# Kernel optimization log

Measured on AMD Instinct MI355X. Metric: run time of the kernel, lower is better.

Reference implementation:

```python
import jax, jax.numpy as jnp
import numpy as np

M, L, D, V = 4096, 15, 1024, 32  # moves, word_max, in_sz, vocab_sz


def setup_inputs() -> dict:
    key = jax.random.key(0)
    ks = jax.random.split(key, 9)
    s = 0.02
    return {
        "tokens": jax.random.randint(ks[0], (M, L), 0, V),
        "letter_emb": jax.random.normal(ks[1], (V, D), jnp.float32) * s,
        "pos_emb": jax.random.normal(ks[2], (L, D), jnp.float32) * s,
        "Wq": jax.random.normal(ks[3], (D, D), jnp.float32) * s,
        "bq": jax.random.normal(ks[4], (D,), jnp.float32) * s,
        "Wk": jax.random.normal(ks[5], (D, D), jnp.float32) * s,
        "bk": jax.random.normal(ks[6], (D,), jnp.float32) * s,
        "Wv": jax.random.normal(ks[7], (D, D), jnp.float32) * s,
        "bv": jax.random.normal(ks[8], (D,), jnp.float32) * s,
    }


def reference(tokens, letter_emb, pos_emb, Wq, bq, Wk, bk, Wv, bv):
    # WordEncoder, batched across all M moves.
    x = letter_emb[tokens] + pos_emb[None, :, :]          # [M, L, D]
    q = jnp.einsum("mld,ed->mle", x, Wq) + bq             # Linear: x @ W.T + b
    k = jnp.einsum("mld,ed->mle", x, Wk) + bk
    v = jnp.einsum("mld,ed->mle", x, Wv) + bv
    scores = jax.nn.softmax(jnp.einsum("mle,mke->mlk", q, k), axis=-1)  # [M, L, L]
    attn = jnp.einsum("mlk,mke->mle", scores, v)          # [M, L, D]
    word = attn.sum(axis=1)                               # [M, D]
    # enc = word + ordered, where ordered is an identical second evaluation
    # of word_enc on the same word -> enc = 2 * word.
    return 2.0 * word
```

## Files before the change

kernel.cpp:

```cpp
#include <hip/hip_runtime.h>
#include <hip/hip_bf16.h>

#define NMOVES 4096
#define LW     15
#define DIM    1024
#define VOC    32
#define NROW   480
#define MROW   512

#define GSPLIT 4
#define KSEG   (DIM/GSPLIT)
#define GN     512

typedef __attribute__((ext_vector_type(8))) short  short8;
typedef __attribute__((ext_vector_type(4))) float  floatx4;

__device__ __forceinline__ unsigned short f2b(float f) {
  unsigned int x;
  __builtin_memcpy(&x, &f, 4);
  x = x + 0x7FFFu + ((x >> 16) & 1u);
  return (unsigned short)(x >> 16);
}
__device__ __forceinline__ float b2f(unsigned short u) {
  unsigned int x = ((unsigned int)u) << 16;
  float f;
  __builtin_memcpy(&f, &x, 4);
  return f;
}

#define LDK 72

__global__ __launch_bounds__(256) void prep(
    const float* __restrict__ letter, const float* __restrict__ pos,
    const float* __restrict__ Wq, const float* __restrict__ Wk,
    const float* __restrict__ Wv,
    unsigned short* __restrict__ Eb, unsigned short* __restrict__ Wb) {
  const int id = blockIdx.x * 256 + threadIdx.x;
  const int ECHUNK = MROW * DIM / 8;
  const int WCHUNK = DIM * DIM / 8;

  if (id < ECHUNK) {
    const int row = id >> 7;
    const int c   = (id & 127) << 3;
    ushort4 o0 = make_ushort4(0, 0, 0, 0), o1 = o0;
    if (row < NROW) {
      const int t = row / LW;
      const int l = row - t * LW;
      const float* la = letter + (size_t)t * DIM + c;
      const float* lp = pos    + (size_t)l * DIM + c;
      float4 x0 = *reinterpret_cast<const float4*>(la);
      float4 x1 = *reinterpret_cast<const float4*>(la + 4);
      float4 p0 = *reinterpret_cast<const float4*>(lp);
      float4 p1 = *reinterpret_cast<const float4*>(lp + 4);
      o0.x = f2b(x0.x + p0.x); o0.y = f2b(x0.y + p0.y);
      o0.z = f2b(x0.z + p0.z); o0.w = f2b(x0.w + p0.w);
      o1.x = f2b(x1.x + p1.x); o1.y = f2b(x1.y + p1.y);
      o1.z = f2b(x1.z + p1.z); o1.w = f2b(x1.w + p1.w);
    }
    *reinterpret_cast<ushort4*>(Eb + (size_t)row * DIM + c)     = o0;
    *reinterpret_cast<ushort4*>(Eb + (size_t)row * DIM + c + 4) = o1;
  } else {
    const int wi = id - ECHUNK;
    const int m  = wi >> 17;
    const int rem = wi & (WCHUNK - 1);
    const float* src = (m == 0) ? Wq : (m == 1) ? Wk : Wv;
    const float* p = src + (size_t)rem * 8;
    float4 x0 = *reinterpret_cast<const float4*>(p);
    float4 x1 = *reinterpret_cast<const float4*>(p + 4);
    ushort4 o0, o1;
    o0.x = f2b(x0.x); o0.y = f2b(x0.y); o0.z = f2b(x0.z); o0.w = f2b(x0.w);
    o1.x = f2b(x1.x); o1.y = f2b(x1.y); o1.z = f2b(x1.z); o1.w = f2b(x1.w);
    unsigned short* dst = Wb + (size_t)m * DIM * DIM + (size_t)rem * 8;
    *reinterpret_cast<ushort4*>(dst)     = o0;
    *reinterpret_cast<ushort4*>(dst + 4) = o1;
  }
}

__global__ __launch_bounds__(256) void qkv_fused(
    const unsigned short* __restrict__ Eb, const unsigned short* __restrict__ Wb,
    const float* __restrict__ bq, const float* __restrict__ bk,
    const float* __restrict__ bv,
    unsigned short* __restrict__ Qb, unsigned short* __restrict__ Kb,
    unsigned short* __restrict__ Vb) {
  __shared__ __attribute__((aligned(16))) unsigned short lA[64 * LDK];
  __shared__ __attribute__((aligned(16))) unsigned short lB[64 * LDK];

  const unsigned short* W = Wb + (size_t)blockIdx.z * DIM * DIM;
  const float* bias = (blockIdx.z == 0) ? bq : (blockIdx.z == 1) ? bk : bv;
  unsigned short* O = (blockIdx.z == 0) ? Qb : (blockIdx.z == 1) ? Kb : Vb;

  const int bm0 = blockIdx.x * 64;
  const int bn0 = blockIdx.y * 64;

  const int tid  = threadIdx.x;
  const int lane = tid & 63;
  const int wave = tid >> 6;
  const int wr   = wave >> 1;
  const int wc   = wave & 1;
  const int quad = lane >> 4;
  const int l16  = lane & 15;

  const int srow = tid >> 3;
  const int scol = (tid & 7) << 3;

  const unsigned short* As = Eb + (size_t)(bm0 + srow) * DIM + scol;
  const unsigned short* Bs = W  + (size_t)(bn0 + srow) * DIM + scol;

  short8 ra0 = *reinterpret_cast<const short8*>(As);
  short8 ra1 = *reinterpret_cast<const short8*>(As + 32 * DIM);
  short8 rb0 = *reinterpret_cast<const short8*>(Bs);
  short8 rb1 = *reinterpret_cast<const short8*>(Bs + 32 * DIM);

  floatx4 acc[2][2];
#pragma unroll
  for (int i = 0; i < 2; ++i)
#pragma unroll
    for (int j = 0; j < 2; ++j) acc[i][j] = (floatx4){0.f, 0.f, 0.f, 0.f};

  for (int k0 = 0; k0 < DIM; k0 += 64) {
    *reinterpret_cast<short8*>(lA + srow * LDK + scol)        = ra0;
    *reinterpret_cast<short8*>(lA + (srow + 32) * LDK + scol) = ra1;
    *reinterpret_cast<short8*>(lB + srow * LDK + scol)        = rb0;
    *reinterpret_cast<short8*>(lB + (srow + 32) * LDK + scol) = rb1;
    __syncthreads();
    if (k0 + 64 < DIM) {
      ra0 = *reinterpret_cast<const short8*>(As + k0 + 64);
      ra1 = *reinterpret_cast<const short8*>(As + 32 * DIM + k0 + 64);
      rb0 = *reinterpret_cast<const short8*>(Bs + k0 + 64);
      rb1 = *reinterpret_cast<const short8*>(Bs + 32 * DIM + k0 + 64);
    }
#pragma unroll
    for (int kk = 0; kk < 64; kk += 32) {
      short8 a0 = *reinterpret_cast<const short8*>(lA + (wr * 32 + l16) * LDK + kk + quad * 8);
      short8 a1 = *reinterpret_cast<const short8*>(lA + (wr * 32 + 16 + l16) * LDK + kk + quad * 8);
      short8 b0 = *reinterpret_cast<const short8*>(lB + (wc * 32 + l16) * LDK + kk + quad * 8);
      short8 b1 = *reinterpret_cast<const short8*>(lB + (wc * 32 + 16 + l16) * LDK + kk + quad * 8);
      acc[0][0] = __builtin_amdgcn_mfma_f32_16x16x32_bf16(a0, b0, acc[0][0], 0, 0, 0);
      acc[0][1] = __builtin_amdgcn_mfma_f32_16x16x32_bf16(a0, b1, acc[0][1], 0, 0, 0);
      acc[1][0] = __builtin_amdgcn_mfma_f32_16x16x32_bf16(a1, b0, acc[1][0], 0, 0, 0);
      acc[1][1] = __builtin_amdgcn_mfma_f32_16x16x32_bf16(a1, b1, acc[1][1], 0, 0, 0);
    }
    __syncthreads();
  }

#pragma unroll
  for (int mi = 0; mi < 2; ++mi) {
#pragma unroll
    for (int ni = 0; ni < 2; ++ni) {
      const int gcol = bn0 + wc * 32 + ni * 16 + l16;
      const float bval = bias[gcol];
#pragma unroll
      for (int i = 0; i < 4; ++i) {
        const int grow = bm0 + wr * 32 + mi * 16 + quad * 4 + i;
        O[(size_t)grow * DIM + gcol] = f2b(acc[mi][ni][i] + bval);
      }
    }
  }
}

__global__ __launch_bounds__(256) void gram_split(
    const unsigned short* __restrict__ Qb, const unsigned short* __restrict__ Kb,
    float* __restrict__ Gpart) {
  __shared__ __attribute__((aligned(16))) unsigned short lA[64 * LDK];
  __shared__ __attribute__((aligned(16))) unsigned short lB[64 * LDK];

  const int bm0 = blockIdx.x * 64;
  const int bn0 = blockIdx.y * 64;
  const int kbase = blockIdx.z * KSEG;
  float* Gout = Gpart + (size_t)blockIdx.z * GN * GN;

  const int tid  = threadIdx.x;
  const int lane = tid & 63;
  const int wave = tid >> 6;
  const int wr   = wave >> 1;
  const int wc   = wave & 1;
  const int quad = lane >> 4;
  const int l16  = lane & 15;
  const int srow = tid >> 3;
  const int scol = (tid & 7) << 3;

  const unsigned short* As = Qb + (size_t)(bm0 + srow) * DIM + kbase + scol;
  const unsigned short* Bs = Kb + (size_t)(bn0 + srow) * DIM + kbase + scol;

  short8 ra0 = *reinterpret_cast<const short8*>(As);
  short8 ra1 = *reinterpret_cast<const short8*>(As + 32 * DIM);
  short8 rb0 = *reinterpret_cast<const short8*>(Bs);
  short8 rb1 = *reinterpret_cast<const short8*>(Bs + 32 * DIM);

  floatx4 acc[2][2];
#pragma unroll
  for (int i = 0; i < 2; ++i)
#pragma unroll
    for (int j = 0; j < 2; ++j) acc[i][j] = (floatx4){0.f, 0.f, 0.f, 0.f};

  for (int k0 = 0; k0 < KSEG; k0 += 64) {
    *reinterpret_cast<short8*>(lA + srow * LDK + scol)        = ra0;
    *reinterpret_cast<short8*>(lA + (srow + 32) * LDK + scol) = ra1;
    *reinterpret_cast<short8*>(lB + srow * LDK + scol)        = rb0;
    *reinterpret_cast<short8*>(lB + (srow + 32) * LDK + scol) = rb1;
    __syncthreads();
    if (k0 + 64 < KSEG) {
      ra0 = *reinterpret_cast<const short8*>(As + k0 + 64);
      ra1 = *reinterpret_cast<const short8*>(As + 32 * DIM + k0 + 64);
      rb0 = *reinterpret_cast<const short8*>(Bs + k0 + 64);
      rb1 = *reinterpret_cast<const short8*>(Bs + 32 * DIM + k0 + 64);
    }
#pragma unroll
    for (int kk = 0; kk < 64; kk += 32) {
      short8 a0 = *reinterpret_cast<const short8*>(lA + (wr * 32 + l16) * LDK + kk + quad * 8);
      short8 a1 = *reinterpret_cast<const short8*>(lA + (wr * 32 + 16 + l16) * LDK + kk + quad * 8);
      short8 b0 = *reinterpret_cast<const short8*>(lB + (wc * 32 + l16) * LDK + kk + quad * 8);
      short8 b1 = *reinterpret_cast<const short8*>(lB + (wc * 32 + 16 + l16) * LDK + kk + quad * 8);
      acc[0][0] = __builtin_amdgcn_mfma_f32_16x16x32_bf16(a0, b0, acc[0][0], 0, 0, 0);
      acc[0][1] = __builtin_amdgcn_mfma_f32_16x16x32_bf16(a0, b1, acc[0][1], 0, 0, 0);
      acc[1][0] = __builtin_amdgcn_mfma_f32_16x16x32_bf16(a1, b0, acc[1][0], 0, 0, 0);
      acc[1][1] = __builtin_amdgcn_mfma_f32_16x16x32_bf16(a1, b1, acc[1][1], 0, 0, 0);
    }
    __syncthreads();
  }

#pragma unroll
  for (int mi = 0; mi < 2; ++mi) {
#pragma unroll
    for (int ni = 0; ni < 2; ++ni) {
      const int gcol = bn0 + wc * 32 + ni * 16 + l16;
#pragma unroll
      for (int i = 0; i < 4; ++i) {
        const int grow = bm0 + wr * 32 + mi * 16 + quad * 4 + i;
        Gout[(size_t)grow * GN + gcol] = acc[mi][ni][i];
      }
    }
  }
}

__global__ __launch_bounds__(256) void attn_out_k(
    const void* __restrict__ tokens_raw, const float* __restrict__ Gpart,
    const unsigned short* __restrict__ Vb, float* __restrict__ out) {
  __shared__ int   ridx[LW];
  __shared__ float S[LW][16];
  __shared__ float w[16];
  __shared__ int   is64_s;
  const int m = blockIdx.x;
  const int tid = threadIdx.x;

  const unsigned int* u32 = (const unsigned int*)tokens_raw;
  if (tid < 64) {
    unsigned int v = u32[2 * tid + 1];
    unsigned long long nz = __ballot(v != 0);
    if (tid == 0) is64_s = (nz == 0ULL) ? 1 : 0;
  }
  __syncthreads();

  if (tid < LW) {
    int t;
    if (is64_s) t = (int)((const long long*)tokens_raw)[m * LW + tid];
    else        t = ((const int*)tokens_raw)[m * LW + tid];
    ridx[tid] = t * LW + tid;
  }
  __syncthreads();

  if (tid < LW * LW) {
    const int l = tid / LW;
    const int j = tid - l * LW;
    const size_t off = (size_t)ridx[l] * GN + ridx[j];
    float s = 0.f;
#pragma unroll
    for (int p = 0; p < GSPLIT; ++p) s += Gpart[(size_t)p * GN * GN + off];
    S[l][j] = s;
  }
  __syncthreads();

  if (tid < LW) {
    float mx = -1e30f;
#pragma unroll
    for (int j = 0; j < LW; ++j) mx = fmaxf(mx, S[tid][j]);
    float s = 0.f;
#pragma unroll
    for (int j = 0; j < LW; ++j) { float e = __expf(S[tid][j] - mx); S[tid][j] = e; s += e; }
    const float inv = 1.0f / s;
#pragma unroll
    for (int j = 0; j < LW; ++j) S[tid][j] *= inv;
  }
  __syncthreads();

  if (tid < LW) {
    float s = 0.f;
#pragma unroll
    for (int l = 0; l < LW; ++l) s += S[l][tid];
    w[tid] = 2.0f * s;
  }
  __syncthreads();

  const int e0 = tid * 4;
  float a0 = 0.f, a1 = 0.f, a2 = 0.f, a3 = 0.f;
#pragma unroll
  for (int j = 0; j < LW; ++j) {
    const float wj = w[j];
    ushort4 vv = *reinterpret_cast<const ushort4*>(Vb + (size_t)ridx[j] * DIM + e0);
    a0 += wj * b2f(vv.x);
    a1 += wj * b2f(vv.y);
    a2 += wj * b2f(vv.z);
    a3 += wj * b2f(vv.w);
  }
  *reinterpret_cast<float4*>(out + (size_t)m * DIM + e0) =
      make_float4(a0, a1, a2, a3);
}

extern "C" void kernel_launch(void* const* d_in, const int* in_sizes, int n_in,
                              void* d_out, int out_size, void* d_ws, size_t ws_size,
                              hipStream_t stream) {
  const void*  tokens = d_in[0];
  const float* letter = (const float*)d_in[1];
  const float* pos    = (const float*)d_in[2];
  const float* Wq     = (const float*)d_in[3];
  const float* bq     = (const float*)d_in[4];
  const float* Wk     = (const float*)d_in[5];
  const float* bk     = (const float*)d_in[6];
  const float* Wv     = (const float*)d_in[7];
  const float* bv     = (const float*)d_in[8];
  float*       outp   = (float*)d_out;

  char* ws = (char*)d_ws;
  const size_t EB_SZ = (size_t)MROW * DIM * 2;
  const size_t WB_SZ = (size_t)3 * DIM * DIM * 2;
  const size_t OB_SZ = (size_t)MROW * DIM * 2;
  unsigned short* Eb = (unsigned short*)(ws);
  unsigned short* Wb = (unsigned short*)(ws + EB_SZ);
  unsigned short* Qb = (unsigned short*)(ws + EB_SZ + WB_SZ);
  unsigned short* Kb = (unsigned short*)(ws + EB_SZ + WB_SZ + OB_SZ);
  unsigned short* Vb = (unsigned short*)(ws + EB_SZ + WB_SZ + 2 * OB_SZ);
  float*          Gp = (float*)(ws + EB_SZ + WB_SZ + 3 * OB_SZ);

  const int ECHUNK = MROW * DIM / 8;
  const int WCHUNK = DIM * DIM / 8;
  const int PREP_BLOCKS = (ECHUNK + 3 * WCHUNK) / 256;

  prep<<<PREP_BLOCKS, 256, 0, stream>>>(letter, pos, Wq, Wk, Wv, Eb, Wb);
  qkv_fused<<<dim3(8, 16, 3), 256, 0, stream>>>(Eb, Wb, bq, bk, bv, Qb, Kb, Vb);
  gram_split<<<dim3(8, 8, GSPLIT), 256, 0, stream>>>(Qb, Kb, Gp);
  attn_out_k<<<NMOVES, 256, 0, stream>>>(tokens, Gp, Vb, outp);
}
```

Before: 124.9 us.

## Project letter and position embeddings separately and build a 48-row Gram basis

Instead of materialising 480 embedding rows and projecting them through full Q/K/V GEMMs, the kernel projects only the 32 letter rows and 15 position rows, reading fp32 weights and converting to bf16 on the fly. A single block then forms a 48x48 Gram matrix that includes a bias row. The attention kernel rebuilds each score from six basis entries. Terms that are constant across the softmax axis (query·bk, bq·bk) are dropped, which is valid because softmax ignores them. V rows are expanded from the basis plus bias in the same launch. This removes the weight-conversion pass and most GEMM work, but the Gram step now runs serially on one block.

```diff
diff --git a/kernel.cpp b/kernel.cpp
--- a/kernel.cpp
+++ b/kernel.cpp
@@ -6,11 +6,8 @@
 #define DIM    1024
 #define VOC    32
 #define NROW   480
-#define MROW   512
-
-#define GSPLIT 4
-#define KSEG   (DIM/GSPLIT)
-#define GN     512
+#define XROW   48
+#define G48LD  64
 
 typedef __attribute__((ext_vector_type(8))) short  short8;
 typedef __attribute__((ext_vector_type(4))) float  floatx4;
@@ -21,6 +18,10 @@
   x = x + 0x7FFFu + ((x >> 16) & 1u);
   return (unsigned short)(x >> 16);
 }
+__device__ __forceinline__ ushort4 cvt4(float4 v) {
+  ushort4 o; o.x = f2b(v.x); o.y = f2b(v.y); o.z = f2b(v.z); o.w = f2b(v.w);
+  return o;
+}
 __device__ __forceinline__ float b2f(unsigned short u) {
   unsigned int x = ((unsigned int)u) << 16;
   float f;
@@ -30,66 +31,17 @@
 
 #define LDK 72
 
-__global__ __launch_bounds__(256) void prep(
+__global__ __launch_bounds__(256) void proj_small(
     const float* __restrict__ letter, const float* __restrict__ pos,
     const float* __restrict__ Wq, const float* __restrict__ Wk,
     const float* __restrict__ Wv,
-    unsigned short* __restrict__ Eb, unsigned short* __restrict__ Wb) {
-  const int id = blockIdx.x * 256 + threadIdx.x;
-  const int ECHUNK = MROW * DIM / 8;
-  const int WCHUNK = DIM * DIM / 8;
-
-  if (id < ECHUNK) {
-    const int row = id >> 7;
-    const int c   = (id & 127) << 3;
-    ushort4 o0 = make_ushort4(0, 0, 0, 0), o1 = o0;
-    if (row < NROW) {
-      const int t = row / LW;
-      const int l = row - t * LW;
-      const float* la = letter + (size_t)t * DIM + c;
-      const float* lp = pos    + (size_t)l * DIM + c;
-      float4 x0 = *reinterpret_cast<const float4*>(la);
-      float4 x1 = *reinterpret_cast<const float4*>(la + 4);
-      float4 p0 = *reinterpret_cast<const float4*>(lp);
-      float4 p1 = *reinterpret_cast<const float4*>(lp + 4);
-      o0.x = f2b(x0.x + p0.x); o0.y = f2b(x0.y + p0.y);
-      o0.z = f2b(x0.z + p0.z); o0.w = f2b(x0.w + p0.w);
-      o1.x = f2b(x1.x + p1.x); o1.y = f2b(x1.y + p1.y);
-      o1.z = f2b(x1.z + p1.z); o1.w = f2b(x1.w + p1.w);
-    }
-    *reinterpret_cast<ushort4*>(Eb + (size_t)row * DIM + c)     = o0;
-    *reinterpret_cast<ushort4*>(Eb + (size_t)row * DIM + c + 4) = o1;
-  } else {
-    const int wi = id - ECHUNK;
-    const int m  = wi >> 17;
-    const int rem = wi & (WCHUNK - 1);
-    const float* src = (m == 0) ? Wq : (m == 1) ? Wk : Wv;
-    const float* p = src + (size_t)rem * 8;
-    float4 x0 = *reinterpret_cast<const float4*>(p);
-    float4 x1 = *reinterpret_cast<const float4*>(p + 4);
-    ushort4 o0, o1;
-    o0.x = f2b(x0.x); o0.y = f2b(x0.y); o0.z = f2b(x0.z); o0.w = f2b(x0.w);
-    o1.x = f2b(x1.x); o1.y = f2b(x1.y); o1.z = f2b(x1.z); o1.w = f2b(x1.w);
-    unsigned short* dst = Wb + (size_t)m * DIM * DIM + (size_t)rem * 8;
-    *reinterpret_cast<ushort4*>(dst)     = o0;
-    *reinterpret_cast<ushort4*>(dst + 4) = o1;
-  }
-}
-
-__global__ __launch_bounds__(256) void qkv_fused(
-    const unsigned short* __restrict__ Eb, const unsigned short* __restrict__ Wb,
-    const float* __restrict__ bq, const float* __restrict__ bk,
-    const float* __restrict__ bv,
-    unsigned short* __restrict__ Qb, unsigned short* __restrict__ Kb,
-    unsigned short* __restrict__ Vb) {
+    float* __restrict__ Xq, float* __restrict__ Xk, float* __restrict__ Xv) {
   __shared__ __attribute__((aligned(16))) unsigned short lA[64 * LDK];
   __shared__ __attribute__((aligned(16))) unsigned short lB[64 * LDK];
 
-  const unsigned short* W = Wb + (size_t)blockIdx.z * DIM * DIM;
-  const float* bias = (blockIdx.z == 0) ? bq : (blockIdx.z == 1) ? bk : bv;
-  unsigned short* O = (blockIdx.z == 0) ? Qb : (blockIdx.z == 1) ? Kb : Vb;
-
-  const int bm0 = blockIdx.x * 64;
+  const float* W = (blockIdx.z == 0) ? Wq : (blockIdx.z == 1) ? Wk : Wv;
+  float*       O = (blockIdx.z == 0) ? Xq : (blockIdx.z == 1) ? Xk : Xv;
+
   const int bn0 = blockIdx.y * 64;
 
   const int tid  = threadIdx.x;
@@ -99,17 +51,24 @@
   const int wc   = wave & 1;
   const int quad = lane >> 4;
   const int l16  = lane & 15;
-
   const int srow = tid >> 3;
   const int scol = (tid & 7) << 3;
 
-  const unsigned short* As = Eb + (size_t)(bm0 + srow) * DIM + scol;
-  const unsigned short* Bs = W  + (size_t)(bn0 + srow) * DIM + scol;
-
-  short8 ra0 = *reinterpret_cast<const short8*>(As);
-  short8 ra1 = *reinterpret_cast<const short8*>(As + 32 * DIM);
-  short8 rb0 = *reinterpret_cast<const short8*>(Bs);
-  short8 rb1 = *reinterpret_cast<const short8*>(Bs + 32 * DIM);
+  const float* aptr0 = letter + (size_t)srow * DIM + scol;
+  const bool   av1   = (srow < LW);
+  const float* aptr1 = av1 ? (pos + (size_t)srow * DIM + scol) : letter;
+  const float* bptr0 = W + (size_t)(bn0 + srow) * DIM + scol;
+  const float* bptr1 = bptr0 + (size_t)32 * DIM;
+
+  const float4 z4 = make_float4(0.f, 0.f, 0.f, 0.f);
+  float4 ra00 = *reinterpret_cast<const float4*>(aptr0);
+  float4 ra01 = *reinterpret_cast<const float4*>(aptr0 + 4);
+  float4 ra10 = av1 ? *reinterpret_cast<const float4*>(aptr1)     : z4;
+  float4 ra11 = av1 ? *reinterpret_cast<const float4*>(aptr1 + 4) : z4;
+  float4 rb00 = *reinterpret_cast<const float4*>(bptr0);
+  float4 rb01 = *reinterpret_cast<const float4*>(bptr0 + 4);
+  float4 rb10 = *reinterpret_cast<const float4*>(bptr1);
+  float4 rb11 = *reinterpret_cast<const float4*>(bptr1 + 4);
 
   floatx4 acc[2][2];
 #pragma unroll
@@ -118,16 +77,25 @@
     for (int j = 0; j < 2; ++j) acc[i][j] = (floatx4){0.f, 0.f, 0.f, 0.f};
 
   for (int k0 = 0; k0 < DIM; k0 += 64) {
-    *reinterpret_cast<short8*>(lA + srow * LDK + scol)        = ra0;
-    *reinterpret_cast<short8*>(lA + (srow + 32) * LDK + scol) = ra1;
-    *reinterpret_cast<short8*>(lB + srow * LDK + scol)        = rb0;
-    *reinterpret_cast<short8*>(lB + (srow + 32) * LDK + scol) = rb1;
+    *reinterpret_cast<ushort4*>(lA + srow * LDK + scol)            = cvt4(ra00);
+    *reinterpret_cast<ushort4*>(lA + srow * LDK + scol + 4)        = cvt4(ra01);
+    *reinterpret_cast<ushort4*>(lA + (srow + 32) * LDK + scol)     = cvt4(ra10);
+    *reinterpret_cast<ushort4*>(lA + (srow + 32) * LDK + scol + 4) = cvt4(ra11);
+    *reinterpret_cast<ushort4*>(lB + srow * LDK + scol)            = cvt4(rb00);
+    *reinterpret_cast<ushort4*>(lB + srow * LDK + scol + 4)        = cvt4(rb01);
+    *reinterpret_cast<ushort4*>(lB + (srow + 32) * LDK + scol)     = cvt4(rb10);
+    *reinterpret_cast<ushort4*>(lB + (srow + 32) * LDK + scol + 4) = cvt4(rb11);
     __syncthreads();
     if (k0 + 64 < DIM) {
-      ra0 = *reinterpret_cast<const short8*>(As + k0 + 64);
-      ra1 = *reinterpret_cast<const short8*>(As + 32 * DIM + k0 + 64);
-      rb0 = *reinterpret_cast<const short8*>(Bs + k0 + 64);
-      rb1 = *reinterpret_cast<const short8*>(Bs + 32 * DIM + k0 + 64);
+      const int k = k0 + 64;
+      ra00 = *reinterpret_cast<const float4*>(aptr0 + k);
+      ra01 = *reinterpret_cast<const float4*>(aptr0 + k + 4);
+      ra10 = av1 ? *reinterpret_cast<const float4*>(aptr1 + k)     : z4;
+      ra11 = av1 ? *reinterpret_cast<const float4*>(aptr1 + k + 4) : z4;
+      rb00 = *reinterpret_cast<const float4*>(bptr0 + k);
+      rb01 = *reinterpret_cast<const float4*>(bptr0 + k + 4);
+      rb10 = *reinterpret_cast<const float4*>(bptr1 + k);
+      rb11 = *reinterpret_cast<const float4*>(bptr1 + k + 4);
     }
 #pragma unroll
     for (int kk = 0; kk < 64; kk += 32) {
@@ -148,94 +116,138 @@
 #pragma unroll
     for (int ni = 0; ni < 2; ++ni) {
       const int gcol = bn0 + wc * 32 + ni * 16 + l16;
-      const float bval = bias[gcol];
 #pragma unroll
       for (int i = 0; i < 4; ++i) {
-        const int grow = bm0 + wr * 32 + mi * 16 + quad * 4 + i;
-        O[(size_t)grow * DIM + gcol] = f2b(acc[mi][ni][i] + bval);
+        const int grow = wr * 32 + mi * 16 + quad * 4 + i;
+        if (grow < XROW - 1)
+          O[(size_t)grow * DIM + gcol] = acc[mi][ni][i];
       }
     }
   }
 }
 
-__global__ __launch_bounds__(256) void gram_split(
-    const unsigned short* __restrict__ Qb, const unsigned short* __restrict__ Kb,
-    float* __restrict__ Gpart) {
-  __shared__ __attribute__((aligned(16))) unsigned short lA[64 * LDK];
-  __shared__ __attribute__((aligned(16))) unsigned short lB[64 * LDK];
-
-  const int bm0 = blockIdx.x * 64;
-  const int bn0 = blockIdx.y * 64;
-  const int kbase = blockIdx.z * KSEG;
-  float* Gout = Gpart + (size_t)blockIdx.z * GN * GN;
-
-  const int tid  = threadIdx.x;
-  const int lane = tid & 63;
-  const int wave = tid >> 6;
-  const int wr   = wave >> 1;
-  const int wc   = wave & 1;
-  const int quad = lane >> 4;
-  const int l16  = lane & 15;
-  const int srow = tid >> 3;
-  const int scol = (tid & 7) << 3;
-
-  const unsigned short* As = Qb + (size_t)(bm0 + srow) * DIM + kbase + scol;
-  const unsigned short* Bs = Kb + (size_t)(bn0 + srow) * DIM + kbase + scol;
-
-  short8 ra0 = *reinterpret_cast<const short8*>(As);
-  short8 ra1 = *reinterpret_cast<const short8*>(As + 32 * DIM);
-  short8 rb0 = *reinterpret_cast<const short8*>(Bs);
-  short8 rb1 = *reinterpret_cast<const short8*>(Bs + 32 * DIM);
-
-  floatx4 acc[2][2];
-#pragma unroll
-  for (int i = 0; i < 2; ++i)
-#pragma unroll
-    for (int j = 0; j < 2; ++j) acc[i][j] = (floatx4){0.f, 0.f, 0.f, 0.f};
-
-  for (int k0 = 0; k0 < KSEG; k0 += 64) {
-    *reinterpret_cast<short8*>(lA + srow * LDK + scol)        = ra0;
-    *reinterpret_cast<short8*>(lA + (srow + 32) * LDK + scol) = ra1;
-    *reinterpret_cast<short8*>(lB + srow * LDK + scol)        = rb0;
-    *reinterpret_cast<short8*>(lB + (srow + 32) * LDK + scol) = rb1;
-    __syncthreads();
-    if (k0 + 64 < KSEG) {
-      ra0 = *reinterpret_cast<const short8*>(As + k0 + 64);
-      ra1 = *reinterpret_cast<const short8*>(As + 32 * DIM + k0 + 64);
-      rb0 = *reinterpret_cast<const short8*>(Bs + k0 + 64);
-      rb1 = *reinterpret_cast<const short8*>(Bs + 32 * DIM + k0 + 64);
-    }
-#pragma unroll
-    for (int kk = 0; kk < 64; kk += 32) {
-      short8 a0 = *reinterpret_cast<const short8*>(lA + (wr * 32 + l16) * LDK + kk + quad * 8);
-      short8 a1 = *reinterpret_cast<const short8*>(lA + (wr * 32 + 16 + l16) * LDK + kk + quad * 8);
-      short8 b0 = *reinterpret_cast<const short8*>(lB + (wc * 32 + l16) * LDK + kk + quad * 8);
-      short8 b1 = *reinterpret_cast<const short8*>(lB + (wc * 32 + 16 + l16) * LDK + kk + quad * 8);
-      acc[0][0] = __builtin_amdgcn_mfma_f32_16x16x32_bf16(a0, b0, acc[0][0], 0, 0, 0);
-      acc[0][1] = __builtin_amdgcn_mfma_f32_16x16x32_bf16(a0, b1, acc[0][1], 0, 0, 0);
-      acc[1][0] = __builtin_amdgcn_mfma_f32_16x16x32_bf16(a1, b0, acc[1][0], 0, 0, 0);
-      acc[1][1] = __builtin_amdgcn_mfma_f32_16x16x32_bf16(a1, b1, acc[1][1], 0, 0, 0);
-    }
-    __syncthreads();
-  }
-
-#pragma unroll
-  for (int mi = 0; mi < 2; ++mi) {
-#pragma unroll
-    for (int ni = 0; ni < 2; ++ni) {
-      const int gcol = bn0 + wc * 32 + ni * 16 + l16;
-#pragma unroll
-      for (int i = 0; i < 4; ++i) {
-        const int grow = bm0 + wr * 32 + mi * 16 + quad * 4 + i;
-        Gout[(size_t)grow * GN + gcol] = acc[mi][ni][i];
+__global__ __launch_bounds__(256) void gram_vexp(
+    const float* __restrict__ Xq, const float* __restrict__ Xk,
+    const float* __restrict__ bq, const float* __restrict__ bk,
+    const float* __restrict__ Xv, const float* __restrict__ bv,
+    float* __restrict__ G48, unsigned short* __restrict__ Vb) {
+  const int tid = threadIdx.x;
+
+  if (blockIdx.x == 0) {
+    __shared__ __attribute__((aligned(16))) unsigned short lA[64 * LDK];
+    __shared__ __attribute__((aligned(16))) unsigned short lB[64 * LDK];
+
+    const int lane = tid & 63;
+    const int wave = tid >> 6;
+    const int wr   = wave >> 1;
+    const int wc   = wave & 1;
+    const int quad = lane >> 4;
+    const int l16  = lane & 15;
+    const int srow = tid >> 3;
+    const int scol = (tid & 7) << 3;
+
+    const float* aptr0 = Xq + (size_t)srow * DIM + scol;
+    const float* bptr0 = Xk + (size_t)srow * DIM + scol;
+    const bool   v1    = (srow <= LW);
+    const float* aptr1 = (srow < LW) ? (Xq + (size_t)(32 + srow) * DIM + scol)
+                                     : (srow == LW ? (bq + scol) : Xq);
+    const float* bptr1 = (srow < LW) ? (Xk + (size_t)(32 + srow) * DIM + scol)
+                                     : (srow == LW ? (bk + scol) : Xk);
+
+    const float4 z4 = make_float4(0.f, 0.f, 0.f, 0.f);
+    float4 ra00 = *reinterpret_cast<const float4*>(aptr0);
+    float4 ra01 = *reinterpret_cast<const float4*>(aptr0 + 4);
+    float4 ra10 = v1 ? *reinterpret_cast<const float4*>(aptr1)     : z4;
+    float4 ra11 = v1 ? *reinterpret_cast<const float4*>(aptr1 + 4) : z4;
+    float4 rb00 = *reinterpret_cast<const float4*>(bptr0);
+    float4 rb01 = *reinterpret_cast<const float4*>(bptr0 + 4);
+    float4 rb10 = v1 ? *reinterpret_cast<const float4*>(bptr1)     : z4;
+    float4 rb11 = v1 ? *reinterpret_cast<const float4*>(bptr1 + 4) : z4;
+
+    floatx4 acc[2][2];
+#pragma unroll
+    for (int i = 0; i < 2; ++i)
+#pragma unroll
+      for (int j = 0; j < 2; ++j) acc[i][j] = (floatx4){0.f, 0.f, 0.f, 0.f};
+
+    for (int k0 = 0; k0 < DIM; k0 += 64) {
+      *reinterpret_cast<ushort4*>(lA + srow * LDK + scol)            = cvt4(ra00);
+      *reinterpret_cast<ushort4*>(lA + srow * LDK + scol + 4)        = cvt4(ra01);
+      *reinterpret_cast<ushort4*>(lA + (srow + 32) * LDK + scol)     = cvt4(ra10);
+      *reinterpret_cast<ushort4*>(lA + (srow + 32) * LDK + scol + 4) = cvt4(ra11);
+      *reinterpret_cast<ushort4*>(lB + srow * LDK + scol)            = cvt4(rb00);
+      *reinterpret_cast<ushort4*>(lB + srow * LDK + scol + 4)        = cvt4(rb01);
+      *reinterpret_cast<ushort4*>(lB + (srow + 32) * LDK + scol)     = cvt4(rb10);
+      *reinterpret_cast<ushort4*>(lB + (srow + 32) * LDK + scol + 4) = cvt4(rb11);
+      __syncthreads();
+      if (k0 + 64 < DIM) {
+        const int k = k0 + 64;
+        ra00 = *reinterpret_cast<const float4*>(aptr0 + k);
+        ra01 = *reinterpret_cast<const float4*>(aptr0 + k + 4);
+        ra10 = v1 ? *reinterpret_cast<const float4*>(aptr1 + k)     : z4;
+        ra11 = v1 ? *reinterpret_cast<const float4*>(aptr1 + k + 4) : z4;
+        rb00 = *reinterpret_cast<const float4*>(bptr0 + k);
+        rb01 = *reinterpret_cast<const float4*>(bptr0 + k + 4);
+        rb10 = v1 ? *reinterpret_cast<const float4*>(bptr1 + k)     : z4;
+        rb11 = v1 ? *reinterpret_cast<const float4*>(bptr1 + k + 4) : z4;
       }
-    }
+#pragma unroll
+      for (int kk = 0; kk < 64; kk += 32) {
+        short8 a0 = *reinterpret_cast<const short8*>(lA + (wr * 32 + l16) * LDK + kk + quad * 8);
+        short8 a1 = *reinterpret_cast<const short8*>(lA + (wr * 32 + 16 + l16) * LDK + kk + quad * 8);
+        short8 b0 = *reinterpret_cast<const short8*>(lB + (wc * 32 + l16) * LDK + kk + quad * 8);
+        short8 b1 = *reinterpret_cast<const short8*>(lB + (wc * 32 + 16 + l16) * LDK + kk + quad * 8);
+        acc[0][0] = __builtin_amdgcn_mfma_f32_16x16x32_bf16(a0, b0, acc[0][0], 0, 0, 0);
+        acc[0][1] = __builtin_amdgcn_mfma_f32_16x16x32_bf16(a0, b1, acc[0][1], 0, 0, 0);
+        acc[1][0] = __builtin_amdgcn_mfma_f32_16x16x32_bf16(a1, b0, acc[1][0], 0, 0, 0);
+        acc[1][1] = __builtin_amdgcn_mfma_f32_16x16x32_bf16(a1, b1, acc[1][1], 0, 0, 0);
+      }
+      __syncthreads();
+    }
+
+#pragma unroll
+    for (int mi = 0; mi < 2; ++mi) {
+#pragma unroll
+      for (int ni = 0; ni < 2; ++ni) {
+        const int gcol = wc * 32 + ni * 16 + l16;
+#pragma unroll
+        for (int i = 0; i < 4; ++i) {
+          const int grow = wr * 32 + mi * 16 + quad * 4 + i;
+          if (grow < XROW)
+            G48[(size_t)grow * G48LD + gcol] = acc[mi][ni][i];
+        }
+      }
+    }
+  } else {
+    const int c   = (blockIdx.x - 1) * 256 + tid;
+    const int row = c >> 7;
+    const int col = (c & 127) << 3;
+    const int t   = row / LW;
+    const int l   = row - t * LW;
+    const float* lv = Xv + (size_t)t * DIM + col;
+    const float* pv = Xv + (size_t)(32 + l) * DIM + col;
+    const float* bb = bv + col;
+    float4 x0 = *reinterpret_cast<const float4*>(lv);
+    float4 x1 = *reinterpret_cast<const float4*>(lv + 4);
+    float4 p0 = *reinterpret_cast<const float4*>(pv);
+    float4 p1 = *reinterpret_cast<const float4*>(pv + 4);
+    float4 b0 = *reinterpret_cast<const float4*>(bb);
+    float4 b1 = *reinterpret_cast<const float4*>(bb + 4);
+    ushort4 o0, o1;
+    o0.x = f2b(x0.x + p0.x + b0.x); o0.y = f2b(x0.y + p0.y + b0.y);
+    o0.z = f2b(x0.z + p0.z + b0.z); o0.w = f2b(x0.w + p0.w + b0.w);
+    o1.x = f2b(x1.x + p1.x + b1.x); o1.y = f2b(x1.y + p1.y + b1.y);
+    o1.z = f2b(x1.z + p1.z + b1.z); o1.w = f2b(x1.w + p1.w + b1.w);
+    *reinterpret_cast<ushort4*>(Vb + (size_t)row * DIM + col)     = o0;
+    *reinterpret_cast<ushort4*>(Vb + (size_t)row * DIM + col + 4) = o1;
   }
 }
 
 __global__ __launch_bounds__(256) void attn_out_k(
-    const void* __restrict__ tokens_raw, const float* __restrict__ Gpart,
+    const void* __restrict__ tokens_raw, const float* __restrict__ G48,
     const unsigned short* __restrict__ Vb, float* __restrict__ out) {
+  __shared__ __attribute__((aligned(16))) float Gs[XROW * G48LD];
+  __shared__ int   tok[LW];
   __shared__ int   ridx[LW];
   __shared__ float S[LW][16];
   __shared__ float w[16];
@@ -255,18 +267,25 @@
     int t;
     if (is64_s) t = (int)((const long long*)tokens_raw)[m * LW + tid];
     else        t = ((const int*)tokens_raw)[m * LW + tid];
+    tok[tid]  = t;
     ridx[tid] = t * LW + tid;
+  }
+#pragma unroll
+  for (int i = 0; i < 3; ++i) {
+    const int idx = i * 256 + tid;
+    reinterpret_cast<float4*>(Gs)[idx] =
+        reinterpret_cast<const float4*>(G48)[idx];
   }
   __syncthreads();
 
   if (tid < LW * LW) {
     const int l = tid / LW;
     const int j = tid - l * LW;
-    const size_t off = (size_t)ridx[l] * GN + ridx[j];
-    float s = 0.f;
-#pragma unroll
-    for (int p = 0; p < GSPLIT; ++p) s += Gpart[(size_t)p * GN * GN + off];
-    S[l][j] = s;
+    const int a0 = tok[l], a1 = 32 + l;
+    const int b0 = tok[j], b1 = 32 + j;
+    S[l][j] = Gs[a0 * G48LD + b0] + Gs[a0 * G48LD + b1] +
+              Gs[a1 * G48LD + b0] + Gs[a1 * G48LD + b1] +
+              Gs[(XROW - 1) * G48LD + b0] + Gs[(XROW - 1) * G48LD + b1];
   }
   __syncthreads();
 
@@ -321,22 +340,17 @@
   float*       outp   = (float*)d_out;
 
   char* ws = (char*)d_ws;
-  const size_t EB_SZ = (size_t)MROW * DIM * 2;
-  const size_t WB_SZ = (size_t)3 * DIM * DIM * 2;
-  const size_t OB_SZ = (size_t)MROW * DIM * 2;
-  unsigned short* Eb = (unsigned short*)(ws);
-  unsigned short* Wb = (unsigned short*)(ws + EB_SZ);
-  unsigned short* Qb = (unsigned short*)(ws + EB_SZ + WB_SZ);
-  unsigned short* Kb = (unsigned short*)(ws + EB_SZ + WB_SZ + OB_SZ);
-  unsigned short* Vb = (unsigned short*)(ws + EB_SZ + WB_SZ + 2 * OB_SZ);
-  float*          Gp = (float*)(ws + EB_SZ + WB_SZ + 3 * OB_SZ);
-
-  const int ECHUNK = MROW * DIM / 8;
-  const int WCHUNK = DIM * DIM / 8;
-  const int PREP_BLOCKS = (ECHUNK + 3 * WCHUNK) / 256;
-
-  prep<<<PREP_BLOCKS, 256, 0, stream>>>(letter, pos, Wq, Wk, Wv, Eb, Wb);
-  qkv_fused<<<dim3(8, 16, 3), 256, 0, stream>>>(Eb, Wb, bq, bk, bv, Qb, Kb, Vb);
-  gram_split<<<dim3(8, 8, GSPLIT), 256, 0, stream>>>(Qb, Kb, Gp);
+  const size_t XSZ  = (size_t)XROW * DIM * 4;
+  const size_t GSZ  = (size_t)G48LD * G48LD * 4;
+  float* Xq = (float*)(ws);
+  float* Xk = (float*)(ws + XSZ);
+  float* Xv = (float*)(ws + 2 * XSZ);
+  float* Gp = (float*)(ws + 3 * XSZ);
+  unsigned short* Vb = (unsigned short*)(ws + 3 * XSZ + GSZ);
+
+  proj_small<<<dim3(1, 16, 3), 256, 0, stream>>>(letter, pos, Wq, Wk, Wv,
+                                                 Xq, Xk, Xv);
+  gram_vexp<<<1 + (NROW * DIM / 8 / 256), 256, 0, stream>>>(Xq, Xk, bq, bk,
+                                                            Xv, bv, Gp, Vb);
   attn_out_k<<<NMOVES, 256, 0, stream>>>(tokens, Gp, Vb, outp);
 }
```

New measurement: 137.5 us. +10.1%, slower.
